# Kernel optimization log

Hardware: AMD Instinct MI355X
Metric: run time of the kernel (lower is better)

Reference implementation:

```python
import jax, jax.numpy as jnp
import numpy as np

N, E, IN, HID, OUT = 50000, 1600000, 64, 32, 32
NEG_SLOPE = 0.2  # PyG GATConv default


def gat_conv(x, src, dst, W, a_src, a_dst, b, n):
    """Single-head PyG-style GATConv (dropout off / eval mode).
    x: [n, in], src/dst: [E+n] (self-loops already appended),
    W: [in, out], a_src/a_dst: [out], b: [out]."""
    h = x @ W                                   # [n, out]
    e_src = (h * a_src).sum(-1)                 # [n]
    e_dst = (h * a_dst).sum(-1)                 # [n]
    alpha = jax.nn.leaky_relu(e_src[src] + e_dst[dst], NEG_SLOPE)  # [Etot]
    amax = jax.ops.segment_max(alpha, dst, num_segments=n)         # per-dst max
    ex = jnp.exp(alpha - amax[dst])
    denom = jax.ops.segment_sum(ex, dst, num_segments=n)
    coef = ex / denom[dst]                      # softmax over incoming edges
    out = jax.ops.segment_sum(h[src] * coef[:, None], dst, num_segments=n)
    return out + b


def branch(x, src, dst, W1, as1, ad1, b1, W2, as2, ad2, b2, lW, lb, n):
    h = jax.nn.relu(gat_conv(x, src, dst, W1, as1, ad1, b1, n))
    h = jax.nn.relu(gat_conv(h, src, dst, W2, as2, ad2, b2, n))
    return h @ lW + lb


def setup_inputs() -> dict:
    key = jax.random.key(0)
    ks = jax.random.split(key, 32)
    inp = {
        "x": jax.random.normal(ks[0], (N, IN), dtype=jnp.float32),
        "edge_index": jax.random.randint(ks[1], (2, E), 0, N, dtype=jnp.int64),
    }
    i = 2
    for p in ("c", "r"):
        dims = [(IN, HID), (HID, HID)]
        for li, (di, do) in enumerate(dims, start=1):
            s = (2.0 / (di + do)) ** 0.5
            inp[f"{p}_W{li}"] = jax.random.normal(ks[i], (di, do), dtype=jnp.float32) * s; i += 1
            inp[f"{p}_as{li}"] = jax.random.normal(ks[i], (do,), dtype=jnp.float32) * 0.1; i += 1
            inp[f"{p}_ad{li}"] = jax.random.normal(ks[i], (do,), dtype=jnp.float32) * 0.1; i += 1
            inp[f"{p}_b{li}"] = jnp.zeros((do,), dtype=jnp.float32); i += 1
        inp[f"{p}_lW"] = jax.random.normal(ks[i], (HID, OUT), dtype=jnp.float32) * (2.0 / (HID + OUT)) ** 0.5; i += 1
        inp[f"{p}_lb"] = jnp.zeros((OUT,), dtype=jnp.float32); i += 1
    return inp


def reference(x, edge_index,
              c_W1, c_as1, c_ad1, c_b1, c_W2, c_as2, c_ad2, c_b2, c_lW, c_lb,
              r_W1, r_as1, r_ad1, r_b1, r_W2, r_as2, r_ad2, r_b2, r_lW, r_lb):
    n = x.shape[0]
    loop = jnp.arange(n, dtype=edge_index.dtype)
    src = jnp.concatenate([edge_index[0], loop])  # add_self_loops=True default
    dst = jnp.concatenate([edge_index[1], loop])
    prob_zero = jax.nn.sigmoid(branch(x, src, dst, c_W1, c_as1, c_ad1, c_b1,
                                      c_W2, c_as2, c_ad2, c_b2, c_lW, c_lb, n))
    res = branch(x, src, dst, r_W1, r_as1, r_ad1, r_b1,
                 r_W2, r_as2, r_ad2, r_b2, r_lW, r_lb, n)
    return (prob_zero, res)
```

## Files before the change

### kernel.cpp

```cpp
#include <hip/hip_runtime.h>
#include <hip/hip_fp16.h>
#include <math.h>

#define NEG_SLOPE 0.2f

#define NBUCK_MAX 200
#define A3_BLOCKS 512
#define WINDOW 20480

typedef __attribute__((ext_vector_type(8))) _Float16 v8h;
typedef __attribute__((ext_vector_type(4))) float v4f;

__device__ __forceinline__ int ntload_i(const int* p) {
    return __builtin_nontemporal_load(p);
}

__global__ void init_kernel(int* __restrict__ bcursor, int* __restrict__ bcount,
                            int nbuck) {
    int t = threadIdx.x;
    if (t < nbuck) { bcursor[t] = t * WINDOW; bcount[t] = 0; }
}

__global__ __launch_bounds__(256)
void bucket_scatter_kernel(const int* __restrict__ ei, int E, int n,
                           int nbuck, int dshift,
                           int* __restrict__ bcursor,
                           int* __restrict__ bcount,
                           uint2* __restrict__ pairs) {
    __shared__ int cnt[NBUCK_MAX];
    __shared__ int lcur[NBUCK_MAX];
    int t = threadIdx.x;
    for (int k = t; k < nbuck; k += 256) cnt[k] = 0;
    __syncthreads();
    int Etot = E + n;
    int chunk = (Etot + gridDim.x - 1) / gridDim.x;
    int s0 = blockIdx.x * chunk;
    int s1 = min(Etot, s0 + chunk);
    for (int i = s0 + t; i < s1; i += 256) {
        int d = (i < E) ? ntload_i(ei + E + i) : (i - E);
        if ((unsigned)d < (unsigned)n) atomicAdd(&cnt[d >> dshift], 1);
    }
    __syncthreads();
    for (int k = t; k < nbuck; k += 256) {
        int c = cnt[k];
        if (c) {
            int r = (c + 15) & ~15;
            lcur[k] = atomicAdd(&bcursor[k], r);
            atomicAdd(&bcount[k], c);
        }
    }
    __syncthreads();
    for (int i = s0 + t; i < s1; i += 256) {
        int s, d;
        if (i < E) { s = ntload_i(ei + i); d = ntload_i(ei + E + i); }
        else       { s = d = i - E; }
        if ((unsigned)d < (unsigned)n) {
            if ((unsigned)s >= (unsigned)n) s = 0;
            int pos = atomicAdd(&lcur[d >> dshift], 1);
            pairs[pos] = make_uint2((unsigned)s, (unsigned)d);
        }
    }
    __syncthreads();
    for (int k = t; k < nbuck; k += 256) {
        int c = cnt[k];
        if (c) {
            int pad = ((c + 15) & ~15) - c;
            int p0 = lcur[k];
            for (int p = 0; p < pad; ++p)
                pairs[p0 + p] = make_uint2(0u, 0xFFFFFFFFu);
        }
    }
}

__global__ void bucket_scan_kernel(const int* __restrict__ bcount,
                                   int* __restrict__ colbase,
                                   int* __restrict__ row_ptr,
                                   int n, int nbuck) {
    __shared__ int sm[256];
    int t = threadIdx.x;
    int v = (t < nbuck) ? bcount[t] : 0;
    sm[t] = v;
    __syncthreads();
    int x = v;
    for (int off = 1; off < 256; off <<= 1) {
        int y = (t >= off) ? sm[t - off] : 0;
        __syncthreads();
        x += y;
        sm[t] = x;
        __syncthreads();
    }
    if (t < nbuck) colbase[t] = x - v;
    if (t == nbuck - 1) row_ptr[n] = x;
}

__global__ __launch_bounds__(256)
void fine_scatter_kernel(const uint2* __restrict__ pairs,
                         const int* __restrict__ bcursor,
                         const int* __restrict__ colbase,
                         int* __restrict__ row_ptr,
                         int* __restrict__ col,
                         int n, int dshift) {
    __shared__ int cnt[256];
    __shared__ int ofs[256];
    int b = blockIdx.x, t = threadIdx.x;
    int dsz = 1 << dshift;
    cnt[t] = 0;
    __syncthreads();
    int p0 = b * WINDOW, p1 = bcursor[b];
    int dstart = b << dshift;
    for (int i = p0 + t; i < p1; i += 256) {
        uint2 p = pairs[i];
        int ld = (int)p.y - dstart;
        if ((int)p.y >= 0 && ld >= 0 && ld < dsz) atomicAdd(&cnt[ld], 1);
    }
    __syncthreads();
    int v = cnt[t];
    ofs[t] = v;
    __syncthreads();
    int x = v;
    for (int off = 1; off < 256; off <<= 1) {
        int y = (t >= off) ? ofs[t - off] : 0;
        __syncthreads();
        x += y;
        ofs[t] = x;
        __syncthreads();
    }
    int excl = x - v;
    int cb = colbase[b];
    int d = dstart + t;
    if (d < n) row_ptr[d] = cb + excl;
    cnt[t] = excl;
    __syncthreads();
    for (int i = p0 + t; i < p1; i += 256) {
        uint2 p = pairs[i];
        int ld = (int)p.y - dstart;
        if ((int)p.y >= 0 && ld >= 0 && ld < dsz) {
            int pos = cb + atomicAdd(&cnt[ld], 1);
            col[pos] = (int)p.x;
        }
    }
}

__global__ __launch_bounds__(256)
void xcast_kernel(const float* __restrict__ x, _Float16* __restrict__ xh,
                  int total4) {
    int i = blockIdx.x * blockDim.x + threadIdx.x;
    if (i >= total4) return;
    float4 v = ((const float4*)x)[i];
    _Float16 o[4] = {(_Float16)v.x, (_Float16)v.y, (_Float16)v.z, (_Float16)v.w};
    ((uint2*)xh)[i] = *(const uint2*)o;
}

__global__ void prep_kernel(const float* __restrict__ cW1, const float* __restrict__ rW1,
                            const float* __restrict__ cas1, const float* __restrict__ cad1,
                            const float* __restrict__ ras1, const float* __restrict__ rad1,
                            const float* __restrict__ cW2, const float* __restrict__ rW2,
                            const float* __restrict__ cas2, const float* __restrict__ cad2,
                            const float* __restrict__ ras2, const float* __restrict__ rad2,
                            const float* __restrict__ clW, const float* __restrict__ rlW,
                            _Float16* __restrict__ WB1,
                            _Float16* __restrict__ WB2,
                            _Float16* __restrict__ WBh) {
    __shared__ float f1s[2][64], f1d[2][64];
    __shared__ float f2s[2][32], f2d[2][32];
    int t = threadIdx.x;
    if (t < 128) {
        int b = t >> 6, k = t & 63;
        const float* W   = b ? rW1 : cW1;
        const float* as_ = b ? ras1 : cas1;
        const float* ad_ = b ? rad1 : cad1;
        float s1 = 0.f, s2 = 0.f;
        for (int f = 0; f < 32; ++f) {
            s1 = fmaf(W[k * 32 + f], as_[f], s1);
            s2 = fmaf(W[k * 32 + f], ad_[f], s2);
        }
        f1s[b][k] = s1;
        f1d[b][k] = s2;
    } else if (t < 192) {
        int b = (t - 128) >> 5, k = (t - 128) & 31;
        const float* W   = b ? rW2 : cW2;
        const float* as_ = b ? ras2 : cas2;
        const float* ad_ = b ? rad2 : cad2;
        float s1 = 0.f, s2 = 0.f;
        for (int f = 0; f < 32; ++f) {
            s1 = fmaf(W[k * 32 + f], as_[f], s1);
            s2 = fmaf(W[k * 32 + f], ad_[f], s2);
        }
        f2s[b][k] = s1;
        f2d[b][k] = s2;
    }
    __syncthreads();
    for (int idx = t; idx < 6144; idx += 256) {
        int blk = idx >> 9;
        int l = (idx >> 3) & 63, j = idx & 7;
        int b = blk / 6, rem = blk % 6, c = rem / 3, tt = rem % 3;
        int k = c * 32 + (l >> 4) * 8 + j;
        int nn = l & 15;
        const float* W = b ? rW1 : cW1;
        float v;
        if (tt < 2) v = W[k * 32 + tt * 16 + nn];
        else v = (nn == 0) ? f1s[b][k] : ((nn == 1) ? f1d[b][k] : 0.f);
        WB1[idx] = (_Float16)v;
    }
    for (int idx = t; idx < 3072; idx += 256) {
        int blk = idx >> 9;
        int l = (idx >> 3) & 63, j = idx & 7;
        int b = blk / 3, tt = blk % 3;
        int k = (l >> 4) * 8 + j;
        int nn = l & 15;
        const float* W = b ? rW2 : cW2;
        float v;
        if (tt < 2) v = W[k * 32 + tt * 16 + nn];
        else v = (nn == 0) ? f2s[b][k] : ((nn == 1) ? f2d[b][k] : 0.f);
        WB2[idx] = (_Float16)v;
    }
    for (int idx = t; idx < 2048; idx += 256) {
        int blk = idx >> 9;
        int l = (idx >> 3) & 63, j = idx & 7;
        int b = blk >> 1, tt = blk & 1;
        int k = (l >> 4) * 8 + j;
        int nn = l & 15;
        const float* W = b ? rlW : clW;
        WBh[idx] = (_Float16)W[k * 32 + tt * 16 + nn];
    }
}

__global__ __launch_bounds__(256)
void t1_mfma_kernel(const _Float16* __restrict__ xh,
                    const _Float16* __restrict__ WB1,
                    __half2* __restrict__ h,
                    float2* __restrict__ es2,
                    float2* __restrict__ ed2, int n) {
    int wave = (blockIdx.x * blockDim.x + threadIdx.x) >> 6;
    int lane = threadIdx.x & 63;
    int ntiles = n >> 4;
    if (wave >= ntiles) return;
    int m0 = wave << 4;
    int quad = lane >> 4, nn = lane & 15;
    const _Float16* arow = xh + (size_t)(m0 + nn) * 64 + quad * 8;
    v8h a0 = *(const v8h*)arow;
    v8h a1 = *(const v8h*)(arow + 32);
    v4f acc[2][3];
#pragma unroll
    for (int b = 0; b < 2; ++b)
#pragma unroll
        for (int tt = 0; tt < 3; ++tt) acc[b][tt] = (v4f){0.f, 0.f, 0.f, 0.f};
#pragma unroll
    for (int b = 0; b < 2; ++b) {
#pragma unroll
        for (int c = 0; c < 2; ++c) {
            v8h av = c ? a1 : a0;
#pragma unroll
            for (int tt = 0; tt < 3; ++tt) {
                v8h wb = *(const v8h*)(WB1 + (((b * 2 + c) * 3 + tt) << 9) + lane * 8);
                acc[b][tt] = __builtin_amdgcn_mfma_f32_16x16x32_f16(av, wb, acc[b][tt], 0, 0, 0);
            }
        }
    }
#pragma unroll
    for (int i = 0; i < 4; ++i) {
        int m = m0 + quad * 4 + i;
        h[(size_t)m * 32 + nn]      = __floats2half2_rn(acc[0][0][i], acc[1][0][i]);
        h[(size_t)m * 32 + 16 + nn] = __floats2half2_rn(acc[0][1][i], acc[1][1][i]);
        if (nn == 0) es2[m] = make_float2(acc[0][2][i], acc[1][2][i]);
        if (nn == 1) ed2[m] = make_float2(acc[0][2][i], acc[1][2][i]);
    }
}

__device__ __forceinline__ void load_a_frag(const __half2* __restrict__ g,
                                            int m0, int nn, int quad,
                                            v8h& aC, v8h& aR) {
    const uint4* gp = (const uint4*)(g + (size_t)(m0 + nn) * 32 + quad * 8);
    uint4 q0 = gp[0], q1 = gp[1];
    unsigned short buf[16];
    *(uint4*)buf = q0;
    *(uint4*)(buf + 8) = q1;
#pragma unroll
    for (int i = 0; i < 8; ++i) {
        ((unsigned short*)&aC)[i] = buf[2 * i];
        ((unsigned short*)&aR)[i] = buf[2 * i + 1];
    }
}

__global__ __launch_bounds__(256)
void t2_mfma_kernel(const __half2* __restrict__ g1,
                    const _Float16* __restrict__ WB2,
                    __half2* __restrict__ h2,
                    float2* __restrict__ es2o,
                    float2* __restrict__ ed2o, int n) {
    int wave = (blockIdx.x * blockDim.x + threadIdx.x) >> 6;
    int lane = threadIdx.x & 63;
    if (wave >= (n >> 4)) return;
    int m0 = wave << 4;
    int quad = lane >> 4, nn = lane & 15;
    v8h aC, aR;
    load_a_frag(g1, m0, nn, quad, aC, aR);
    v4f acc[2][3];
#pragma unroll
    for (int b = 0; b < 2; ++b)
#pragma unroll
        for (int tt = 0; tt < 3; ++tt) acc[b][tt] = (v4f){0.f, 0.f, 0.f, 0.f};
#pragma unroll
    for (int b = 0; b < 2; ++b) {
        v8h av = b ? aR : aC;
#pragma unroll
        for (int tt = 0; tt < 3; ++tt) {
            v8h wb = *(const v8h*)(WB2 + ((b * 3 + tt) << 9) + lane * 8);
            acc[b][tt] = __builtin_amdgcn_mfma_f32_16x16x32_f16(av, wb, acc[b][tt], 0, 0, 0);
        }
    }
#pragma unroll
    for (int i = 0; i < 4; ++i) {
        int m = m0 + quad * 4 + i;
        h2[(size_t)m * 32 + nn]      = __floats2half2_rn(acc[0][0][i], acc[1][0][i]);
        h2[(size_t)m * 32 + 16 + nn] = __floats2half2_rn(acc[0][1][i], acc[1][1][i]);
        if (nn == 0) es2o[m] = make_float2(acc[0][2][i], acc[1][2][i]);
        if (nn == 1) ed2o[m] = make_float2(acc[0][2][i], acc[1][2][i]);
    }
}

__global__ __launch_bounds__(256)
void head_mfma_kernel(const __half2* __restrict__ g2,
                      const _Float16* __restrict__ WBh,
                      const float* __restrict__ clb,
                      const float* __restrict__ rlb,
                      float* __restrict__ out, int n) {
    int wave = (blockIdx.x * blockDim.x + threadIdx.x) >> 6;
    int lane = threadIdx.x & 63;
    if (wave >= (n >> 4)) return;
    int m0 = wave << 4;
    int quad = lane >> 4, nn = lane & 15;
    v8h aC, aR;
    load_a_frag(g2, m0, nn, quad, aC, aR);
    v4f acc[2][2];
#pragma unroll
    for (int b = 0; b < 2; ++b)
#pragma unroll
        for (int tt = 0; tt < 2; ++tt) acc[b][tt] = (v4f){0.f, 0.f, 0.f, 0.f};
#pragma unroll
    for (int b = 0; b < 2; ++b) {
        v8h av = b ? aR : aC;
#pragma unroll
        for (int tt = 0; tt < 2; ++tt) {
            v8h wb = *(const v8h*)(WBh + ((b * 2 + tt) << 9) + lane * 8);
            acc[b][tt] = __builtin_amdgcn_mfma_f32_16x16x32_f16(av, wb, acc[b][tt], 0, 0, 0);
        }
    }
    float lb0c = clb[nn], lb1c = clb[16 + nn];
    float lb0r = rlb[nn], lb1r = rlb[16 + nn];
#pragma unroll
    for (int i = 0; i < 4; ++i) {
        int m = m0 + quad * 4 + i;
        float y0 = acc[0][0][i] + lb0c;
        float y1 = acc[0][1][i] + lb1c;
        out[(size_t)m * 32 + nn]      = 1.f / (1.f + __expf(-y0));
        out[(size_t)m * 32 + 16 + nn] = 1.f / (1.f + __expf(-y1));
        out[(size_t)n * 32 + (size_t)m * 32 + nn]      = acc[1][0][i] + lb0r;
        out[(size_t)n * 32 + (size_t)m * 32 + 16 + nn] = acc[1][1][i] + lb1r;
    }
}

__global__ __launch_bounds__(256, 8)
void agg_kernel(const int* __restrict__ row_ptr,
                const int* __restrict__ col,
                const __half2* __restrict__ h,
                const float2* __restrict__ es2,
                const float2* __restrict__ ed2,
                const float* __restrict__ bc,
                const float* __restrict__ br,
                __half2* __restrict__ gout, int n) {
    int grp = (blockIdx.x * blockDim.x + threadIdx.x) >> 5;
    int lane = threadIdx.x & 31;
    int sub = lane >> 2;
    int fq  = lane & 3;
    if (grp >= n) return;
    int d = grp;
    int beg = row_ptr[d], end = row_ptr[d + 1];
    float2 edv = ed2[d];
    float accC[8], accR[8];
#pragma unroll
    for (int i = 0; i < 8; ++i) { accC[i] = 0.f; accR[i] = 0.f; }
    float lc = 0.f, lr = 0.f;
    for (int base = beg; base + sub < end; base += 8) {
        int e = base + sub;
        int s = ntload_i(col + e);
        float2 ev = es2[s];
        float tc = ev.x + edv.x, tr = ev.y + edv.y;
        tc = (tc > 0.f) ? tc : NEG_SLOPE * tc;
        tr = (tr > 0.f) ? tr : NEG_SLOPE * tr;
        float exc = __expf(tc), exr = __expf(tr);
        lc += exc; lr += exr;
        const uint4* rp = (const uint4*)(h + ((size_t)s << 5));
        uint4 q0 = rp[2 * fq];
        uint4 q1 = rp[2 * fq + 1];
        const __half2* hp0 = (const __half2*)&q0;
        const __half2* hp1 = (const __half2*)&q1;
#pragma unroll
        for (int i = 0; i < 4; ++i) {
            float2 v0 = __half22float2(hp0[i]);
            float2 v1 = __half22float2(hp1[i]);
            accC[i]     = fmaf(v0.x, exc, accC[i]);
            accR[i]     = fmaf(v0.y, exr, accR[i]);
            accC[4 + i] = fmaf(v1.x, exc, accC[4 + i]);
            accR[4 + i] = fmaf(v1.y, exr, accR[4 + i]);
        }
    }
#pragma unroll
    for (int off = 4; off <= 16; off <<= 1) {
        lc += __shfl_xor(lc, off, 32);
        lr += __shfl_xor(lr, off, 32);
#pragma unroll
        for (int i = 0; i < 8; ++i) {
            accC[i] += __shfl_xor(accC[i], off, 32);
            accR[i] += __shfl_xor(accR[i], off, 32);
        }
    }
    if (sub == 0) {
        float ilc = 1.f / lc, ilr = 1.f / lr;
        __half2 o[8];
#pragma unroll
        for (int i = 0; i < 8; ++i) {
            float gc = fmaxf(accC[i] * ilc + bc[fq * 8 + i], 0.f);
            float gr = fmaxf(accR[i] * ilr + br[fq * 8 + i], 0.f);
            o[i] = __floats2half2_rn(gc, gr);
        }
        uint4* dst = (uint4*)(gout + ((size_t)d << 5) + fq * 8);
        dst[0] = *(const uint4*)&o[0];
        dst[1] = *(const uint4*)&o[4];
    }
}

extern "C" void kernel_launch(void* const* d_in, const int* in_sizes, int n_in,
                              void* d_out, int out_size, void* d_ws, size_t ws_size,
                              hipStream_t stream) {
    const float* x = (const float*)d_in[0];
    const int* ei = (const int*)d_in[1];
    const int N = in_sizes[0] / 64;
    const int E = in_sizes[1] / 2;
    const int Etot = E + N;

    const float* cW1  = (const float*)d_in[2];
    const float* cas1 = (const float*)d_in[3];
    const float* cad1 = (const float*)d_in[4];
    const float* cb1  = (const float*)d_in[5];
    const float* cW2  = (const float*)d_in[6];
    const float* cas2 = (const float*)d_in[7];
    const float* cad2 = (const float*)d_in[8];
    const float* cb2  = (const float*)d_in[9];
    const float* clW  = (const float*)d_in[10];
    const float* clb  = (const float*)d_in[11];
    const float* rW1  = (const float*)d_in[12];
    const float* ras1 = (const float*)d_in[13];
    const float* rad1 = (const float*)d_in[14];
    const float* rb1  = (const float*)d_in[15];
    const float* rW2  = (const float*)d_in[16];
    const float* ras2 = (const float*)d_in[17];
    const float* rad2 = (const float*)d_in[18];
    const float* rb2  = (const float*)d_in[19];
    const float* rlW  = (const float*)d_in[20];
    const float* rlb  = (const float*)d_in[21];

    int dshift = 8;
    while (((N + (1 << dshift) - 1) >> dshift) > NBUCK_MAX) ++dshift;
    const int nbuck = (N + (1 << dshift) - 1) >> dshift;

    char* w = (char*)d_ws;
    size_t off = 0;
    auto alloc = [&](size_t bytes) {
        void* p = w + off;
        off = (off + bytes + 255) & ~(size_t)255;
        return p;
    };
    int*       row_ptr = (int*)alloc((size_t)(N + 1) * 4);
    int*       colbase = (int*)alloc(NBUCK_MAX * 4);
    int*       bcount  = (int*)alloc(NBUCK_MAX * 4);
    int*       bcursor = (int*)alloc(NBUCK_MAX * 4);
    int*       col     = (int*)alloc((size_t)Etot * 4);
    uint2*     pairs   = (uint2*)alloc((size_t)NBUCK_MAX * WINDOW * 8);
    __half2*   h       = (__half2*)alloc((size_t)N * 32 * 4);
    __half2*   g       = (__half2*)alloc((size_t)N * 32 * 4);
    float2*    esA     = (float2*)alloc((size_t)N * 8);
    float2*    edA     = (float2*)alloc((size_t)N * 8);
    float2*    esB     = (float2*)alloc((size_t)N * 8);
    float2*    edB     = (float2*)alloc((size_t)N * 8);
    _Float16*  xh      = (_Float16*)alloc((size_t)N * 64 * 2);
    _Float16*  WB1     = (_Float16*)alloc(6144 * 2);
    _Float16*  WB2     = (_Float16*)alloc(3072 * 2);
    _Float16*  WBh     = (_Float16*)alloc(2048 * 2);
    (void)ws_size;

    float* out = (float*)d_out;
    const int node_blocks = (N * 32 + 255) / 256;
    const int xc_blocks   = (N * 64 / 4 + 255) / 256;
    const int mfma_blocks = ((N >> 4) * 64 + 255) / 256;

    init_kernel<<<1, 256, 0, stream>>>(bcursor, bcount, nbuck);
    xcast_kernel<<<xc_blocks, 256, 0, stream>>>(x, xh, N * 64 / 4);
    prep_kernel<<<1, 256, 0, stream>>>(cW1, rW1, cas1, cad1, ras1, rad1,
                                       cW2, rW2, cas2, cad2, ras2, rad2,
                                       clW, rlW, WB1, WB2, WBh);
    bucket_scatter_kernel<<<A3_BLOCKS, 256, 0, stream>>>(ei, E, N, nbuck, dshift,
                                                         bcursor, bcount, pairs);
    bucket_scan_kernel<<<1, 256, 0, stream>>>(bcount, colbase, row_ptr, N, nbuck);
    fine_scatter_kernel<<<nbuck, 256, 0, stream>>>(pairs, bcursor, colbase,
                                                   row_ptr, col, N, dshift);

    t1_mfma_kernel<<<mfma_blocks, 256, 0, stream>>>(xh, WB1, h, esA, edA, N);
    agg_kernel<<<node_blocks, 256, 0, stream>>>(
        row_ptr, col, h, esA, edA, cb1, rb1, g, N);

    t2_mfma_kernel<<<mfma_blocks, 256, 0, stream>>>(g, WB2, h, esB, edB, N);
    agg_kernel<<<node_blocks, 256, 0, stream>>>(
        row_ptr, col, h, esB, edB, cb2, rb2, g, N);
    head_mfma_kernel<<<mfma_blocks, 256, 0, stream>>>(g, WBh, clb, rlb, out, N);
}
```

Measured before the change: 285.6 us.

## Replace two-level bucket CSR build with global-atomic histogram, scan and scatter

Swaps the bucketed two-pass CSR construction, which staged edges in a padded pairs buffer, for a direct per-node degree histogram with global atomics, a three-kernel prefix scan, and an atomic-cursor scatter into col. After the scatter, rptr holds end offsets, so aggregation reads beg from rptr[d-1]. Degree zeroing is folded into the cast kernel. This drops the 8-byte pairs buffer traffic, but the scatter now uses heavily contended global atomics with random writes, and neighbour order within a row becomes nondeterministic.

```diff
diff --git a/kernel.cpp b/kernel.cpp
--- a/kernel.cpp
+++ b/kernel.cpp
@@ -4,10 +4,6 @@
 
 #define NEG_SLOPE 0.2f
 
-#define NBUCK_MAX 200
-#define A3_BLOCKS 512
-#define WINDOW 20480
-
 typedef __attribute__((ext_vector_type(8))) _Float16 v8h;
 typedef __attribute__((ext_vector_type(4))) float v4f;
 
@@ -15,70 +11,47 @@
     return __builtin_nontemporal_load(p);
 }
 
-__global__ void init_kernel(int* __restrict__ bcursor, int* __restrict__ bcount,
-                            int nbuck) {
-    int t = threadIdx.x;
-    if (t < nbuck) { bcursor[t] = t * WINDOW; bcount[t] = 0; }
-}
-
-__global__ __launch_bounds__(256)
-void bucket_scatter_kernel(const int* __restrict__ ei, int E, int n,
-                           int nbuck, int dshift,
-                           int* __restrict__ bcursor,
-                           int* __restrict__ bcount,
-                           uint2* __restrict__ pairs) {
-    __shared__ int cnt[NBUCK_MAX];
-    __shared__ int lcur[NBUCK_MAX];
-    int t = threadIdx.x;
-    for (int k = t; k < nbuck; k += 256) cnt[k] = 0;
+__global__ __launch_bounds__(256)
+void xcast_kernel(const float* __restrict__ x, _Float16* __restrict__ xh,
+                  int total4, int n, int* __restrict__ deg) {
+    int i = blockIdx.x * blockDim.x + threadIdx.x;
+    if (i < n) deg[i] = 0;
+    if (i >= total4) return;
+    float4 v = ((const float4*)x)[i];
+    _Float16 o[4] = {(_Float16)v.x, (_Float16)v.y, (_Float16)v.z, (_Float16)v.w};
+    ((uint2*)xh)[i] = *(const uint2*)o;
+}
+
+__global__ __launch_bounds__(256)
+void hist_kernel(const int* __restrict__ ei, int E, int n,
+                 int* __restrict__ deg) {
+    int total = E + n;
+    int stride = gridDim.x * 256;
+    for (int i = blockIdx.x * 256 + threadIdx.x; i < total; i += stride) {
+        int d = (i < E) ? ntload_i(ei + E + i) : (i - E);
+        if ((unsigned)d < (unsigned)n) atomicAdd(&deg[d], 1);
+    }
+}
+
+__global__ void scan_reduce_kernel(const int* __restrict__ deg,
+                                   int* __restrict__ bsum, int n) {
+    __shared__ int sm[256];
+    int b = blockIdx.x, t = threadIdx.x;
+    int d = b * 256 + t;
+    sm[t] = (d < n) ? deg[d] : 0;
     __syncthreads();
-    int Etot = E + n;
-    int chunk = (Etot + gridDim.x - 1) / gridDim.x;
-    int s0 = blockIdx.x * chunk;
-    int s1 = min(Etot, s0 + chunk);
-    for (int i = s0 + t; i < s1; i += 256) {
-        int d = (i < E) ? ntload_i(ei + E + i) : (i - E);
-        if ((unsigned)d < (unsigned)n) atomicAdd(&cnt[d >> dshift], 1);
-    }
-    __syncthreads();
-    for (int k = t; k < nbuck; k += 256) {
-        int c = cnt[k];
-        if (c) {
-            int r = (c + 15) & ~15;
-            lcur[k] = atomicAdd(&bcursor[k], r);
-            atomicAdd(&bcount[k], c);
-        }
-    }
-    __syncthreads();
-    for (int i = s0 + t; i < s1; i += 256) {
-        int s, d;
-        if (i < E) { s = ntload_i(ei + i); d = ntload_i(ei + E + i); }
-        else       { s = d = i - E; }
-        if ((unsigned)d < (unsigned)n) {
-            if ((unsigned)s >= (unsigned)n) s = 0;
-            int pos = atomicAdd(&lcur[d >> dshift], 1);
-            pairs[pos] = make_uint2((unsigned)s, (unsigned)d);
-        }
-    }
-    __syncthreads();
-    for (int k = t; k < nbuck; k += 256) {
-        int c = cnt[k];
-        if (c) {
-            int pad = ((c + 15) & ~15) - c;
-            int p0 = lcur[k];
-            for (int p = 0; p < pad; ++p)
-                pairs[p0 + p] = make_uint2(0u, 0xFFFFFFFFu);
-        }
-    }
-}
-
-__global__ void bucket_scan_kernel(const int* __restrict__ bcount,
-                                   int* __restrict__ colbase,
-                                   int* __restrict__ row_ptr,
-                                   int n, int nbuck) {
+    for (int off = 128; off; off >>= 1) {
+        if (t < off) sm[t] += sm[t + off];
+        __syncthreads();
+    }
+    if (t == 0) bsum[b] = sm[0];
+}
+
+__global__ void scan_base_kernel(const int* __restrict__ bsum,
+                                 int* __restrict__ bbase, int nseg) {
     __shared__ int sm[256];
     int t = threadIdx.x;
-    int v = (t < nbuck) ? bcount[t] : 0;
+    int v = (t < nseg) ? bsum[t] : 0;
     sm[t] = v;
     __syncthreads();
     int x = v;
@@ -89,66 +62,44 @@
         sm[t] = x;
         __syncthreads();
     }
-    if (t < nbuck) colbase[t] = x - v;
-    if (t == nbuck - 1) row_ptr[n] = x;
-}
-
-__global__ __launch_bounds__(256)
-void fine_scatter_kernel(const uint2* __restrict__ pairs,
-                         const int* __restrict__ bcursor,
-                         const int* __restrict__ colbase,
-                         int* __restrict__ row_ptr,
-                         int* __restrict__ col,
-                         int n, int dshift) {
-    __shared__ int cnt[256];
-    __shared__ int ofs[256];
+    if (t < nseg) bbase[t] = x - v;
+}
+
+__global__ void scan_write_kernel(const int* __restrict__ deg,
+                                  const int* __restrict__ bbase,
+                                  int* __restrict__ rptr, int n) {
+    __shared__ int sm[256];
     int b = blockIdx.x, t = threadIdx.x;
-    int dsz = 1 << dshift;
-    cnt[t] = 0;
-    __syncthreads();
-    int p0 = b * WINDOW, p1 = bcursor[b];
-    int dstart = b << dshift;
-    for (int i = p0 + t; i < p1; i += 256) {
-        uint2 p = pairs[i];
-        int ld = (int)p.y - dstart;
-        if ((int)p.y >= 0 && ld >= 0 && ld < dsz) atomicAdd(&cnt[ld], 1);
-    }
-    __syncthreads();
-    int v = cnt[t];
-    ofs[t] = v;
+    int d = b * 256 + t;
+    int v = (d < n) ? deg[d] : 0;
+    sm[t] = v;
     __syncthreads();
     int x = v;
     for (int off = 1; off < 256; off <<= 1) {
-        int y = (t >= off) ? ofs[t - off] : 0;
+        int y = (t >= off) ? sm[t - off] : 0;
         __syncthreads();
         x += y;
-        ofs[t] = x;
+        sm[t] = x;
         __syncthreads();
     }
-    int excl = x - v;
-    int cb = colbase[b];
-    int d = dstart + t;
-    if (d < n) row_ptr[d] = cb + excl;
-    cnt[t] = excl;
-    __syncthreads();
-    for (int i = p0 + t; i < p1; i += 256) {
-        uint2 p = pairs[i];
-        int ld = (int)p.y - dstart;
-        if ((int)p.y >= 0 && ld >= 0 && ld < dsz) {
-            int pos = cb + atomicAdd(&cnt[ld], 1);
-            col[pos] = (int)p.x;
-        }
-    }
-}
-
-__global__ __launch_bounds__(256)
-void xcast_kernel(const float* __restrict__ x, _Float16* __restrict__ xh,
-                  int total4) {
-    int i = blockIdx.x * blockDim.x + threadIdx.x;
-    if (i >= total4) return;
-    float4 v = ((const float4*)x)[i];
-    _Float16 o[4] = {(_Float16)v.x, (_Float16)v.y, (_Float16)v.z, (_Float16)v.w};
-    ((uint2*)xh)[i] = *(const uint2*)o;
+    if (d < n) rptr[d] = bbase[b] + x - v;
+}
+
+__global__ __launch_bounds__(256)
+void scatter_kernel(const int* __restrict__ ei, int E, int n,
+                    int* __restrict__ rptr, int* __restrict__ col) {
+    int total = E + n;
+    int stride = gridDim.x * 256;
+    for (int i = blockIdx.x * 256 + threadIdx.x; i < total; i += stride) {
+        int s, d;
+        if (i < E) { s = ntload_i(ei + i); d = ntload_i(ei + E + i); }
+        else       { s = d = i - E; }
+        if ((unsigned)d < (unsigned)n) {
+            if ((unsigned)s >= (unsigned)n) s = 0;
+            int pos = atomicAdd(&rptr[d], 1);
+            col[pos] = s;
+        }
+    }
 }
 
 __global__ void prep_kernel(const float* __restrict__ cW1, const float* __restrict__ rW1,
@@ -361,7 +312,7 @@
 }
 
 __global__ __launch_bounds__(256, 8)
-void agg_kernel(const int* __restrict__ row_ptr,
+void agg_kernel(const int* __restrict__ rptr,
                 const int* __restrict__ col,
                 const __half2* __restrict__ h,
                 const float2* __restrict__ es2,
@@ -375,7 +326,8 @@
     int fq  = lane & 3;
     if (grp >= n) return;
     int d = grp;
-    int beg = row_ptr[d], end = row_ptr[d + 1];
+    int beg = d ? rptr[d - 1] : 0;
+    int end = rptr[d];
     float2 edv = ed2[d];
     float accC[8], accR[8];
 #pragma unroll
@@ -460,10 +412,6 @@
     const float* rlW  = (const float*)d_in[20];
     const float* rlb  = (const float*)d_in[21];
 
-    int dshift = 8;
-    while (((N + (1 << dshift) - 1) >> dshift) > NBUCK_MAX) ++dshift;
-    const int nbuck = (N + (1 << dshift) - 1) >> dshift;
-
     char* w = (char*)d_ws;
     size_t off = 0;
     auto alloc = [&](size_t bytes) {
@@ -471,46 +419,47 @@
         off = (off + bytes + 255) & ~(size_t)255;
         return p;
     };
-    int*       row_ptr = (int*)alloc((size_t)(N + 1) * 4);
-    int*       colbase = (int*)alloc(NBUCK_MAX * 4);
-    int*       bcount  = (int*)alloc(NBUCK_MAX * 4);
-    int*       bcursor = (int*)alloc(NBUCK_MAX * 4);
-    int*       col     = (int*)alloc((size_t)Etot * 4);
-    uint2*     pairs   = (uint2*)alloc((size_t)NBUCK_MAX * WINDOW * 8);
-    __half2*   h       = (__half2*)alloc((size_t)N * 32 * 4);
-    __half2*   g       = (__half2*)alloc((size_t)N * 32 * 4);
-    float2*    esA     = (float2*)alloc((size_t)N * 8);
-    float2*    edA     = (float2*)alloc((size_t)N * 8);
-    float2*    esB     = (float2*)alloc((size_t)N * 8);
-    float2*    edB     = (float2*)alloc((size_t)N * 8);
-    _Float16*  xh      = (_Float16*)alloc((size_t)N * 64 * 2);
-    _Float16*  WB1     = (_Float16*)alloc(6144 * 2);
-    _Float16*  WB2     = (_Float16*)alloc(3072 * 2);
-    _Float16*  WBh     = (_Float16*)alloc(2048 * 2);
+    int*       rptr  = (int*)alloc((size_t)N * 4);
+    int*       deg   = (int*)alloc((size_t)N * 4);
+    int*       bsum  = (int*)alloc(256 * 4);
+    int*       bbase = (int*)alloc(256 * 4);
+    int*       col   = (int*)alloc((size_t)Etot * 4);
+    __half2*   h     = (__half2*)alloc((size_t)N * 32 * 4);
+    __half2*   g     = (__half2*)alloc((size_t)N * 32 * 4);
+    float2*    esA   = (float2*)alloc((size_t)N * 8);
+    float2*    edA   = (float2*)alloc((size_t)N * 8);
+    float2*    esB   = (float2*)alloc((size_t)N * 8);
+    float2*    edB   = (float2*)alloc((size_t)N * 8);
+    _Float16*  xh    = (_Float16*)alloc((size_t)N * 64 * 2);
+    _Float16*  WB1   = (_Float16*)alloc(6144 * 2);
+    _Float16*  WB2   = (_Float16*)alloc(3072 * 2);
+    _Float16*  WBh   = (_Float16*)alloc(2048 * 2);
     (void)ws_size;
 
     float* out = (float*)d_out;
     const int node_blocks = (N * 32 + 255) / 256;
     const int xc_blocks   = (N * 64 / 4 + 255) / 256;
     const int mfma_blocks = ((N >> 4) * 64 + 255) / 256;
-
-    init_kernel<<<1, 256, 0, stream>>>(bcursor, bcount, nbuck);
-    xcast_kernel<<<xc_blocks, 256, 0, stream>>>(x, xh, N * 64 / 4);
+    int eb = (Etot + 255) / 256;
+    const int eblocks = (eb < 2048) ? eb : 2048;
+    const int nseg = (N + 255) / 256;
+
+    xcast_kernel<<<xc_blocks, 256, 0, stream>>>(x, xh, N * 64 / 4, N, deg);
     prep_kernel<<<1, 256, 0, stream>>>(cW1, rW1, cas1, cad1, ras1, rad1,
                                        cW2, rW2, cas2, cad2, ras2, rad2,
                                        clW, rlW, WB1, WB2, WBh);
-    bucket_scatter_kernel<<<A3_BLOCKS, 256, 0, stream>>>(ei, E, N, nbuck, dshift,
-                                                         bcursor, bcount, pairs);
-    bucket_scan_kernel<<<1, 256, 0, stream>>>(bcount, colbase, row_ptr, N, nbuck);
-    fine_scatter_kernel<<<nbuck, 256, 0, stream>>>(pairs, bcursor, colbase,
-                                                   row_ptr, col, N, dshift);
+    hist_kernel<<<eblocks, 256, 0, stream>>>(ei, E, N, deg);
+    scan_reduce_kernel<<<nseg, 256, 0, stream>>>(deg, bsum, N);
+    scan_base_kernel<<<1, 256, 0, stream>>>(bsum, bbase, nseg);
+    scan_write_kernel<<<nseg, 256, 0, stream>>>(deg, bbase, rptr, N);
+    scatter_kernel<<<eblocks, 256, 0, stream>>>(ei, E, N, rptr, col);
 
     t1_mfma_kernel<<<mfma_blocks, 256, 0, stream>>>(xh, WB1, h, esA, edA, N);
     agg_kernel<<<node_blocks, 256, 0, stream>>>(
-        row_ptr, col, h, esA, edA, cb1, rb1, g, N);
+        rptr, col, h, esA, edA, cb1, rb1, g, N);
 
     t2_mfma_kernel<<<mfma_blocks, 256, 0, stream>>>(g, WB2, h, esB, edB, N);
     agg_kernel<<<node_blocks, 256, 0, stream>>>(
-        row_ptr, col, h, esB, edB, cb2, rb2, g, N);
+        rptr, col, h, esB, edB, cb2, rb2, g, N);
     head_mfma_kernel<<<mfma_blocks, 256, 0, stream>>>(g, WBh, clb, rlb, out, N);
 }
```

Measured after the change: 415.9 us. 45.6% more time.

## Rebuild CSR construction as exact two-pass partition with packed 32-bit pairs

Applied to the files above, without the earlier changes.

Replaces the windowed bucket scatter with a count pass, a prefix scan and a write pass, so each edge partition lands at an exact offset with no padding or fixed windows. Each edge becomes one 32-bit word holding the 16-bit source and the local destination. This halves pair traffic for the fine stage. Buckets shrink to 128 destinations, which gives the fine kernel more blocks, and zeroing the bucket counts is folded into the cast kernel to drop a launch. The cost is a second read of the destination indices, and the packing assumes node ids fit in 16 bits.

```diff
diff --git a/kernel.cpp b/kernel.cpp
--- a/kernel.cpp
+++ b/kernel.cpp
@@ -4,9 +4,10 @@
 
 #define NEG_SLOPE 0.2f
 
-#define NBUCK_MAX 200
-#define A3_BLOCKS 512
-#define WINDOW 20480
+#define DSHIFT 7
+#define DSZ 128
+#define NBUCK_MAX 512
+#define PART_BLOCKS 256
 
 typedef __attribute__((ext_vector_type(8))) _Float16 v8h;
 typedef __attribute__((ext_vector_type(4))) float v4f;
@@ -15,20 +16,21 @@
     return __builtin_nontemporal_load(p);
 }
 
-__global__ void init_kernel(int* __restrict__ bcursor, int* __restrict__ bcount,
-                            int nbuck) {
-    int t = threadIdx.x;
-    if (t < nbuck) { bcursor[t] = t * WINDOW; bcount[t] = 0; }
-}
-
-__global__ __launch_bounds__(256)
-void bucket_scatter_kernel(const int* __restrict__ ei, int E, int n,
-                           int nbuck, int dshift,
-                           int* __restrict__ bcursor,
-                           int* __restrict__ bcount,
-                           uint2* __restrict__ pairs) {
+__global__ __launch_bounds__(256)
+void xcast_kernel(const float* __restrict__ x, _Float16* __restrict__ xh,
+                  int total4, int* __restrict__ bcount) {
+    int i = blockIdx.x * blockDim.x + threadIdx.x;
+    if (i < NBUCK_MAX) bcount[i] = 0;
+    if (i >= total4) return;
+    float4 v = ((const float4*)x)[i];
+    _Float16 o[4] = {(_Float16)v.x, (_Float16)v.y, (_Float16)v.z, (_Float16)v.w};
+    ((uint2*)xh)[i] = *(const uint2*)o;
+}
+
+__global__ __launch_bounds__(256)
+void part_count_kernel(const int* __restrict__ ei, int E, int n, int nbuck,
+                       int* __restrict__ bcount) {
     __shared__ int cnt[NBUCK_MAX];
-    __shared__ int lcur[NBUCK_MAX];
     int t = threadIdx.x;
     for (int k = t; k < nbuck; k += 256) cnt[k] = 0;
     __syncthreads();
@@ -38,16 +40,58 @@
     int s1 = min(Etot, s0 + chunk);
     for (int i = s0 + t; i < s1; i += 256) {
         int d = (i < E) ? ntload_i(ei + E + i) : (i - E);
-        if ((unsigned)d < (unsigned)n) atomicAdd(&cnt[d >> dshift], 1);
+        if ((unsigned)d < (unsigned)n) atomicAdd(&cnt[d >> DSHIFT], 1);
     }
     __syncthreads();
     for (int k = t; k < nbuck; k += 256) {
         int c = cnt[k];
-        if (c) {
-            int r = (c + 15) & ~15;
-            lcur[k] = atomicAdd(&bcursor[k], r);
-            atomicAdd(&bcount[k], c);
-        }
+        if (c) atomicAdd(&bcount[k], c);
+    }
+}
+
+__global__ void bucket_scan_kernel(const int* __restrict__ bcount,
+                                   int* __restrict__ colbase,
+                                   int* __restrict__ pcur,
+                                   int* __restrict__ rptr,
+                                   int n, int nbuck) {
+    __shared__ int sm[512];
+    int t = threadIdx.x;
+    int v = (t < nbuck) ? bcount[t] : 0;
+    sm[t] = v;
+    __syncthreads();
+    int x = v;
+    for (int off = 1; off < 512; off <<= 1) {
+        int y = (t >= off) ? sm[t - off] : 0;
+        __syncthreads();
+        x += y;
+        sm[t] = x;
+        __syncthreads();
+    }
+    if (t < nbuck) { colbase[t] = x - v; pcur[t] = x - v; }
+    if (t == nbuck - 1) rptr[n] = x;
+}
+
+__global__ __launch_bounds__(256)
+void part_write_kernel(const int* __restrict__ ei, int E, int n, int nbuck,
+                       int* __restrict__ pcur,
+                       unsigned* __restrict__ pairs) {
+    __shared__ int cnt[NBUCK_MAX];
+    __shared__ int lcur[NBUCK_MAX];
+    int t = threadIdx.x;
+    for (int k = t; k < nbuck; k += 256) cnt[k] = 0;
+    __syncthreads();
+    int Etot = E + n;
+    int chunk = (Etot + gridDim.x - 1) / gridDim.x;
+    int s0 = blockIdx.x * chunk;
+    int s1 = min(Etot, s0 + chunk);
+    for (int i = s0 + t; i < s1; i += 256) {
+        int d = (i < E) ? ntload_i(ei + E + i) : (i - E);
+        if ((unsigned)d < (unsigned)n) atomicAdd(&cnt[d >> DSHIFT], 1);
+    }
+    __syncthreads();
+    for (int k = t; k < nbuck; k += 256) {
+        int c = cnt[k];
+        if (c) lcur[k] = atomicAdd(&pcur[k], c);
     }
     __syncthreads();
     for (int i = s0 + t; i < s1; i += 256) {
@@ -56,99 +100,49 @@
         else       { s = d = i - E; }
         if ((unsigned)d < (unsigned)n) {
             if ((unsigned)s >= (unsigned)n) s = 0;
-            int pos = atomicAdd(&lcur[d >> dshift], 1);
-            pairs[pos] = make_uint2((unsigned)s, (unsigned)d);
-        }
-    }
-    __syncthreads();
-    for (int k = t; k < nbuck; k += 256) {
-        int c = cnt[k];
-        if (c) {
-            int pad = ((c + 15) & ~15) - c;
-            int p0 = lcur[k];
-            for (int p = 0; p < pad; ++p)
-                pairs[p0 + p] = make_uint2(0u, 0xFFFFFFFFu);
-        }
-    }
-}
-
-__global__ void bucket_scan_kernel(const int* __restrict__ bcount,
-                                   int* __restrict__ colbase,
-                                   int* __restrict__ row_ptr,
-                                   int n, int nbuck) {
-    __shared__ int sm[256];
-    int t = threadIdx.x;
-    int v = (t < nbuck) ? bcount[t] : 0;
-    sm[t] = v;
+            int pos = atomicAdd(&lcur[d >> DSHIFT], 1);
+            pairs[pos] = (unsigned)s | ((unsigned)(d & (DSZ - 1)) << 16);
+        }
+    }
+}
+
+__global__ __launch_bounds__(256)
+void fine_kernel(const unsigned* __restrict__ pairs,
+                 const int* __restrict__ colbase,
+                 const int* __restrict__ bcount,
+                 int* __restrict__ rptr,
+                 int* __restrict__ col, int n) {
+    __shared__ int cnt[DSZ];
+    __shared__ int ofs[DSZ];
+    int b = blockIdx.x, t = threadIdx.x;
+    int p0 = colbase[b], p1 = p0 + bcount[b];
+    if (t < DSZ) cnt[t] = 0;
+    __syncthreads();
+    for (int i = p0 + t; i < p1; i += 256)
+        atomicAdd(&cnt[pairs[i] >> 16], 1);
+    __syncthreads();
+    int v = (t < DSZ) ? cnt[t] : 0;
+    if (t < DSZ) ofs[t] = v;
     __syncthreads();
     int x = v;
-    for (int off = 1; off < 256; off <<= 1) {
-        int y = (t >= off) ? sm[t - off] : 0;
+    for (int off = 1; off < DSZ; off <<= 1) {
+        int y = (t >= off && t < DSZ) ? ofs[t - off] : 0;
         __syncthreads();
-        x += y;
-        sm[t] = x;
+        if (t < DSZ) { x += y; ofs[t] = x; }
         __syncthreads();
     }
-    if (t < nbuck) colbase[t] = x - v;
-    if (t == nbuck - 1) row_ptr[n] = x;
-}
-
-__global__ __launch_bounds__(256)
-void fine_scatter_kernel(const uint2* __restrict__ pairs,
-                         const int* __restrict__ bcursor,
-                         const int* __restrict__ colbase,
-                         int* __restrict__ row_ptr,
-                         int* __restrict__ col,
-                         int n, int dshift) {
-    __shared__ int cnt[256];
-    __shared__ int ofs[256];
-    int b = blockIdx.x, t = threadIdx.x;
-    int dsz = 1 << dshift;
-    cnt[t] = 0;
-    __syncthreads();
-    int p0 = b * WINDOW, p1 = bcursor[b];
-    int dstart = b << dshift;
+    int d0 = b << DSHIFT;
+    if (t < DSZ) {
+        int start = p0 + x - v;
+        if (d0 + t < n) rptr[d0 + t] = start;
+        cnt[t] = start;
+    }
+    __syncthreads();
     for (int i = p0 + t; i < p1; i += 256) {
-        uint2 p = pairs[i];
-        int ld = (int)p.y - dstart;
-        if ((int)p.y >= 0 && ld >= 0 && ld < dsz) atomicAdd(&cnt[ld], 1);
-    }
-    __syncthreads();
-    int v = cnt[t];
-    ofs[t] = v;
-    __syncthreads();
-    int x = v;
-    for (int off = 1; off < 256; off <<= 1) {
-        int y = (t >= off) ? ofs[t - off] : 0;
-        __syncthreads();
-        x += y;
-        ofs[t] = x;
-        __syncthreads();
-    }
-    int excl = x - v;
-    int cb = colbase[b];
-    int d = dstart + t;
-    if (d < n) row_ptr[d] = cb + excl;
-    cnt[t] = excl;
-    __syncthreads();
-    for (int i = p0 + t; i < p1; i += 256) {
-        uint2 p = pairs[i];
-        int ld = (int)p.y - dstart;
-        if ((int)p.y >= 0 && ld >= 0 && ld < dsz) {
-            int pos = cb + atomicAdd(&cnt[ld], 1);
-            col[pos] = (int)p.x;
-        }
-    }
-}
-
-__global__ __launch_bounds__(256)
-void xcast_kernel(const float* __restrict__ x, _Float16* __restrict__ xh,
-                  int total4) {
-    int i = blockIdx.x * blockDim.x + threadIdx.x;
-    if (i >= total4) return;
-    float4 v = ((const float4*)x)[i];
-    _Float16 o[4] = {(_Float16)v.x, (_Float16)v.y, (_Float16)v.z, (_Float16)v.w};
-    ((uint2*)xh)[i] = *(const uint2*)o;
+        unsigned u = pairs[i];
+        int pos = atomicAdd(&cnt[u >> 16], 1);
+        col[pos] = (int)(u & 0xFFFFu);
+    }
 }
 
 __global__ void prep_kernel(const float* __restrict__ cW1, const float* __restrict__ rW1,
@@ -361,7 +355,7 @@
 }
 
 __global__ __launch_bounds__(256, 8)
-void agg_kernel(const int* __restrict__ row_ptr,
+void agg_kernel(const int* __restrict__ rptr,
                 const int* __restrict__ col,
                 const __half2* __restrict__ h,
                 const float2* __restrict__ es2,
@@ -375,7 +369,7 @@
     int fq  = lane & 3;
     if (grp >= n) return;
     int d = grp;
-    int beg = row_ptr[d], end = row_ptr[d + 1];
+    int beg = rptr[d], end = rptr[d + 1];
     float2 edv = ed2[d];
     float accC[8], accR[8];
 #pragma unroll
@@ -460,9 +454,7 @@
     const float* rlW  = (const float*)d_in[20];
     const float* rlb  = (const float*)d_in[21];
 
-    int dshift = 8;
-    while (((N + (1 << dshift) - 1) >> dshift) > NBUCK_MAX) ++dshift;
-    const int nbuck = (N + (1 << dshift) - 1) >> dshift;
+    const int nbuck = (N + DSZ - 1) >> DSHIFT;
 
     char* w = (char*)d_ws;
     size_t off = 0;
@@ -471,12 +463,12 @@
         off = (off + bytes + 255) & ~(size_t)255;
         return p;
     };
-    int*       row_ptr = (int*)alloc((size_t)(N + 1) * 4);
+    int*       rptr    = (int*)alloc((size_t)(N + 1) * 4);
+    int*       bcount  = (int*)alloc(NBUCK_MAX * 4);
     int*       colbase = (int*)alloc(NBUCK_MAX * 4);
-    int*       bcount  = (int*)alloc(NBUCK_MAX * 4);
-    int*       bcursor = (int*)alloc(NBUCK_MAX * 4);
+    int*       pcur    = (int*)alloc(NBUCK_MAX * 4);
     int*       col     = (int*)alloc((size_t)Etot * 4);
-    uint2*     pairs   = (uint2*)alloc((size_t)NBUCK_MAX * WINDOW * 8);
+    unsigned*  pairs   = (unsigned*)alloc((size_t)Etot * 4);
     __half2*   h       = (__half2*)alloc((size_t)N * 32 * 4);
     __half2*   g       = (__half2*)alloc((size_t)N * 32 * 4);
     float2*    esA     = (float2*)alloc((size_t)N * 8);
@@ -494,23 +486,21 @@
     const int xc_blocks   = (N * 64 / 4 + 255) / 256;
     const int mfma_blocks = ((N >> 4) * 64 + 255) / 256;
 
-    init_kernel<<<1, 256, 0, stream>>>(bcursor, bcount, nbuck);
-    xcast_kernel<<<xc_blocks, 256, 0, stream>>>(x, xh, N * 64 / 4);
+    xcast_kernel<<<xc_blocks, 256, 0, stream>>>(x, xh, N * 64 / 4, bcount);
     prep_kernel<<<1, 256, 0, stream>>>(cW1, rW1, cas1, cad1, ras1, rad1,
                                        cW2, rW2, cas2, cad2, ras2, rad2,
                                        clW, rlW, WB1, WB2, WBh);
-    bucket_scatter_kernel<<<A3_BLOCKS, 256, 0, stream>>>(ei, E, N, nbuck, dshift,
-                                                         bcursor, bcount, pairs);
-    bucket_scan_kernel<<<1, 256, 0, stream>>>(bcount, colbase, row_ptr, N, nbuck);
-    fine_scatter_kernel<<<nbuck, 256, 0, stream>>>(pairs, bcursor, colbase,
-                                                   row_ptr, col, N, dshift);
+    part_count_kernel<<<PART_BLOCKS, 256, 0, stream>>>(ei, E, N, nbuck, bcount);
+    bucket_scan_kernel<<<1, 512, 0, stream>>>(bcount, colbase, pcur, rptr, N, nbuck);
+    part_write_kernel<<<PART_BLOCKS, 256, 0, stream>>>(ei, E, N, nbuck, pcur, pairs);
+    fine_kernel<<<nbuck, 256, 0, stream>>>(pairs, colbase, bcount, rptr, col, N);
 
     t1_mfma_kernel<<<mfma_blocks, 256, 0, stream>>>(xh, WB1, h, esA, edA, N);
     agg_kernel<<<node_blocks, 256, 0, stream>>>(
-        row_ptr, col, h, esA, edA, cb1, rb1, g, N);
+        rptr, col, h, esA, edA, cb1, rb1, g, N);
 
     t2_mfma_kernel<<<mfma_blocks, 256, 0, stream>>>(g, WB2, h, esB, edB, N);
     agg_kernel<<<node_blocks, 256, 0, stream>>>(
-        row_ptr, col, h, esB, edB, cb2, rb2, g, N);
+        rptr, col, h, esB, edB, cb2, rb2, g, N);
     head_mfma_kernel<<<mfma_blocks, 256, 0, stream>>>(g, WBh, clb, rlb, out, N);
 }
```

Result: faster. 278.8 us (-2.4%).
